# Kernel tuning notes

Hardware: AMD Instinct MI355X
Metric: run time of the kernel (lower is better)

## Reference

```python
import jax, jax.numpy as jnp
import numpy as np

B, S, D, H = 8, 2048, 64, 4
Dh = D // H  # head_dim = 16


def setup_inputs() -> dict:
    key = jax.random.key(0)
    k1, k2, k3, k4 = jax.random.split(key, 4)
    x = jax.random.normal(k1, (B, S, D), jnp.float32)
    # Linear weights stored torch-style as [out_features, in_features]
    W_qkv = jax.random.normal(k2, (3 * D, D), jnp.float32) * 0.125
    W_proj = jax.random.normal(k3, (D, D), jnp.float32) * 0.125
    b_proj = jnp.zeros((D,), jnp.float32)
    # Ragged structure: random valid length per sample, causal + padding mask
    lens = jax.random.randint(k4, (B,), S // 4, S + 1)
    pos = jnp.arange(S)
    key_valid = pos[None, :] < lens[:, None]          # [B, S]
    causal = pos[:, None] >= pos[None, :]             # [S, S]
    attn_mask = (causal[None, :, :] & key_valid[:, None, :])[:, None, :, :]  # [B,1,S,S], True=attend
    return {"x": x, "attn_mask": attn_mask, "W_qkv": W_qkv, "W_proj": W_proj, "b_proj": b_proj}


def reference(x, attn_mask, W_qkv, W_proj, b_proj):
    b, s, d = x.shape
    # fused QKV projection (qkv_bias=False)
    qkv = x @ W_qkv.T                                  # [B, S, 3D]
    qkv = qkv.reshape(b, s, 3, H, Dh).transpose(2, 0, 3, 1, 4)  # [3, B, H, S, Dh]
    q, k, v = qkv[0], qkv[1], qkv[2]
    scale = 1.0 / jnp.sqrt(jnp.asarray(Dh, x.dtype))
    scores = jnp.einsum('bhqd,bhkd->bhqk', q, k) * scale  # [B, H, S, S]
    neg = jnp.asarray(jnp.finfo(scores.dtype).min, scores.dtype)
    scores = jnp.where(attn_mask, scores, neg)
    attn = jax.nn.softmax(scores, axis=-1)
    ctx = jnp.einsum('bhqk,bhkd->bhqd', attn, v)       # [B, H, S, Dh]
    ctx = ctx.transpose(0, 2, 1, 3).reshape(b, s, d)   # [B, S, D]
    return ctx @ W_proj.T + b_proj
```

## Files before the change

### kernel.cpp

```cpp
#include <hip/hip_runtime.h>
#include <hip/hip_bf16.h>

typedef __attribute__((ext_vector_type(4))) float f32x4;
typedef __attribute__((ext_vector_type(16))) float f32x16;
typedef __attribute__((ext_vector_type(8))) short bf16x8;
typedef __attribute__((ext_vector_type(4))) short bf16x4;

#define SEQ 2048
#define NH 4
#define DH 16

#define WS_LEN 0
#define WS_WP  1024
#define WS_Q   65536
#define WS_K   (WS_Q + 2097152)
#define WS_V   (WS_K + 2097152)

#define MFMA16 __builtin_amdgcn_mfma_f32_16x16x32_bf16
#define MFMA32 __builtin_amdgcn_mfma_f32_32x32x16_bf16

__device__ __forceinline__ short f2bf(float f){
  __hip_bfloat16 h = __float2bfloat16(f);
  return __builtin_bit_cast(short, h);
}

__device__ __forceinline__ bf16x8 pack8(f32x4 a, f32x4 b){
  bf16x8 r;
  r[0]=f2bf(a[0]); r[1]=f2bf(a[1]); r[2]=f2bf(a[2]); r[3]=f2bf(a[3]);
  r[4]=f2bf(b[0]); r[5]=f2bf(b[1]); r[6]=f2bf(b[2]); r[7]=f2bf(b[3]);
  return r;
}

__global__ __launch_bounds__(256) void qkv_prep_kernel(const float* __restrict__ x,
                                                       const unsigned char* __restrict__ mask,
                                                       const float* __restrict__ wqkv,
                                                       const float* __restrict__ wproj,
                                                       unsigned char* __restrict__ ws){
  const int tid = threadIdx.x;
  if (blockIdx.x == 256){
    if (blockIdx.y == 1){
      short* wp = (short*)(ws + WS_WP);
      for (int i = tid; i < 64*64; i += 256) wp[i] = f2bf(wproj[i]);
      return;
    }
    const unsigned w0 = *(const unsigned*)mask;
    const int mode = (mask[2048] != 0) ? 0 : ((w0 == 1u) ? 1 : ((w0 == 0x3f800000u) ? 2 : 0));
    __shared__ int cnts[8];
    if (tid < 8) cnts[tid] = 0;
    __syncthreads();
    const int b = tid >> 5, j = tid & 31;
    const long long rowbase = (long long)b * SEQ * SEQ + (long long)(SEQ-1) * SEQ;
    int c = 0;
    if (mode == 0){
      const unsigned* mw = (const unsigned*)(mask + rowbase);
      for (int k = j; k < SEQ/4; k += 32){
        unsigned v = mw[k];
        c += (v & 0xffu ? 1:0) + (v & 0xff00u ? 1:0) + (v & 0xff0000u ? 1:0) + (v & 0xff000000u ? 1:0);
      }
    } else if (mode == 1){
      for (int k = j; k < SEQ; k += 32) c += ((const int*)mask)[rowbase + k] != 0;
    } else {
      for (int k = j; k < SEQ; k += 32) c += ((const float*)mask)[rowbase + k] != 0.0f;
    }
    atomicAdd(&cnts[b], c);
    __syncthreads();
    if (tid < 8) ((int*)ws)[tid] = cnts[tid];
    return;
  }

  const int lane = tid & 63;
  const int wv   = tid >> 6;
  const int c    = lane & 15;
  const int g    = lane >> 4;
  const int T0   = blockIdx.x * 64 + wv * 16;
  const f32x4 z = {0.f, 0.f, 0.f, 0.f};

  bf16x8 aw[2];
  {
    const float* xr = x + (long long)(T0 + c) * 64 + g * 8;
    #pragma unroll
    for (int w = 0; w < 2; ++w){
      f32x4 lo = *(const f32x4*)(xr + w*32);
      f32x4 hi = *(const f32x4*)(xr + w*32 + 4);
      aw[w] = pack8(lo, hi);
    }
  }

  const int tokbase = T0 + g*4;
  const int b = tokbase >> 11;
  const int sbase = tokbase & (SEQ-1);
  short* Qd = (short*)(ws + WS_Q);
  short* Kd = (short*)(ws + WS_K);
  short* Vd = (short*)(ws + WS_V);

  #pragma unroll
  for (int oi = 0; oi < 6; ++oi){
    const int ot = blockIdx.y * 6 + oi;
    const float* wr = wqkv + (ot*16 + c) * 64 + g * 8;
    bf16x8 b0 = pack8(*(const f32x4*)(wr),      *(const f32x4*)(wr + 4));
    bf16x8 b1 = pack8(*(const f32x4*)(wr + 32), *(const f32x4*)(wr + 36));
    f32x4 acc = z;
    acc = MFMA16(aw[0], b0, acc, 0, 0, 0);
    acc = MFMA16(aw[1], b1, acc, 0, 0, 0);
    if (ot < 4){
      short* dst = Qd + ((long long)(b*NH + ot) * SEQ) * DH + c;
      #pragma unroll
      for (int r = 0; r < 4; ++r)
        dst[(long long)(sbase + r) * DH] = f2bf(acc[r] * (0.25f * 1.44269504f));
    } else if (ot < 8){
      short* dst = Kd + ((long long)(b*NH + (ot-4)) * SEQ) * DH + c;
      #pragma unroll
      for (int r = 0; r < 4; ++r)
        dst[(long long)(sbase + r) * DH] = f2bf(acc[r]);
    } else {
      bf16x4 pk;
      #pragma unroll
      for (int r = 0; r < 4; ++r) pk[r] = f2bf(acc[r]);
      *(bf16x4*)(Vd + ((long long)(b*NH + (ot-8)) * DH + c) * SEQ + sbase) = pk;
    }
  }
}

__global__ __launch_bounds__(512, 4) void attn_kernel(const unsigned char* __restrict__ ws,
                                                      const float* __restrict__ bproj,
                                                      float* __restrict__ out){
  const int tid  = threadIdx.x;
  const int lane = tid & 63;
  const int wv   = tid >> 6;
  const int h    = wv & 3;
  const int half = wv >> 2;
  const int c    = lane & 15;
  const int g    = lane >> 4;
  const int ql   = lane & 31;
  const int hi   = lane >> 5;
  const int L    = blockIdx.x;
  const int b    = L & 7;
  const int u    = L >> 3;
  const int t    = (u < 32) ? (2*u) : (63 - 2*(u - 32));
  const int q0   = t * 32;
  const int len  = ((const int*)ws)[b];
  const long long bh = (long long)(b*NH + h);
  const short* Q  = (const short*)(ws + WS_Q) + bh * SEQ * DH;
  const short* K  = (const short*)(ws + WS_K) + bh * SEQ * DH;
  const short* Vt = (const short*)(ws + WS_V) + bh * DH * SEQ;
  const short* Wp = (const short*)(ws + WS_WP);

  __shared__ __align__(16) unsigned char smem[78848];
  float* CMB = (float*)(smem + 65536);
  float* LSB = (float*)(smem + 74240);
  const unsigned pb   = (unsigned)wv * 8192;
  const unsigned CTXB = 74752;
  const f32x4 z  = {0.f,0.f,0.f,0.f};
  const f32x16 z16 = {0.f,0.f,0.f,0.f,0.f,0.f,0.f,0.f,0.f,0.f,0.f,0.f,0.f,0.f,0.f,0.f};

  const bf16x8 qf = *(const bf16x8*)(Q + (q0 + ql)*DH + hi*8);

  f32x4 acc[2] = {z, z};
  f32x4 lsv = z;
  const int kcount = min(q0 + 32, len);
  const int nkt  = (kcount + 63) >> 6;
  const int icnt = min(q0 >> 6, len >> 6);
  const int nh0  = nkt >> 1;
  const int kb   = half ? nh0 : 0;
  const int ke   = half ? nkt : nh0;
  const int qg   = q0 + ql;
  const unsigned swq  = (unsigned)(ql & 7) << 4;
  const unsigned sw   = (unsigned)(c & 7) << 4;

  auto qkexp = [&](int tt, bf16x8 (&kk)[2]){
    const int k0 = tt * 64;
    const bool nomask = tt < icnt;
    const unsigned rowb = pb + ((unsigned)(tt & 1) << 12) + (unsigned)ql*128;
    #pragma unroll
    for (int kb32 = 0; kb32 < 2; ++kb32){
      f32x16 st = MFMA32(kk[kb32], qf, z16, 0, 0, 0);
      #pragma unroll
      for (int grp = 0; grp < 4; ++grp){
        const int keybase = kb32*32 + grp*8 + hi*4;
        float p0, p1, p2, p3;
        {
          float e0 = __builtin_amdgcn_exp2f(st[grp*4 + 0]);
          float e1 = __builtin_amdgcn_exp2f(st[grp*4 + 1]);
          float e2 = __builtin_amdgcn_exp2f(st[grp*4 + 2]);
          float e3 = __builtin_amdgcn_exp2f(st[grp*4 + 3]);
          if (!nomask){
            const int k = k0 + keybase;
            e0 = (k   <= qg && k   < len) ? e0 : 0.f;
            e1 = (k+1 <= qg && k+1 < len) ? e1 : 0.f;
            e2 = (k+2 <= qg && k+2 < len) ? e2 : 0.f;
            e3 = (k+3 <= qg && k+3 < len) ? e3 : 0.f;
          }
          p0 = e0; p1 = e1; p2 = e2; p3 = e3;
        }
        lsv[0] += p0; lsv[1] += p1; lsv[2] += p2; lsv[3] += p3;
        uint2 pk;
        pk.x = __builtin_amdgcn_perm(__builtin_bit_cast(unsigned, p1),
                                     __builtin_bit_cast(unsigned, p0), 0x07060302u);
        pk.y = __builtin_amdgcn_perm(__builtin_bit_cast(unsigned, p3),
                                     __builtin_bit_cast(unsigned, p2), 0x07060302u);
        *(uint2*)&smem[rowb + ((unsigned)(keybase*2) ^ swq)] = pk;
      }
    }
  };

  bf16x8 knx[2], vcur[2], vnx[2], knn[2], vnn[2];
  if (kb < ke){
    const int k0 = kb * 64;
    bf16x8 k0f[2];
    k0f[0] = *(const bf16x8*)(K + (k0 + ql)*DH + hi*8);
    k0f[1] = *(const bf16x8*)(K + (k0 + 32 + ql)*DH + hi*8);
    vcur[0] = *(const bf16x8*)(Vt + c*SEQ + k0 + g*8);
    vcur[1] = *(const bf16x8*)(Vt + c*SEQ + k0 + 32 + g*8);
    qkexp(kb, k0f);
    if (kb + 1 < ke){
      const int k1 = k0 + 64;
      knx[0] = *(const bf16x8*)(K + (k1 + ql)*DH + hi*8);
      knx[1] = *(const bf16x8*)(K + (k1 + 32 + ql)*DH + hi*8);
      vnx[0] = *(const bf16x8*)(Vt + c*SEQ + k1 + g*8);
      vnx[1] = *(const bf16x8*)(Vt + c*SEQ + k1 + 32 + g*8);
    }
  }

  for (int kt = kb; kt < ke; ++kt){
    const unsigned bufr = pb + ((unsigned)(kt & 1) << 12);
    bf16x8 pa[2][2];
    #pragma unroll
    for (int qb = 0; qb < 2; ++qb)
      #pragma unroll
      for (int w = 0; w < 2; ++w)
        pa[qb][w] = *(const bf16x8*)&smem[bufr + (qb*16 + c)*128 + ((unsigned)(w*64 + g*16) ^ sw)];

    if (kt + 1 < ke){
      if (kt + 2 < ke){
        const int k2 = (kt + 2) * 64;
        knn[0] = *(const bf16x8*)(K + (k2 + ql)*DH + hi*8);
        knn[1] = *(const bf16x8*)(K + (k2 + 32 + ql)*DH + hi*8);
        vnn[0] = *(const bf16x8*)(Vt + c*SEQ + k2 + g*8);
        vnn[1] = *(const bf16x8*)(Vt + c*SEQ + k2 + 32 + g*8);
      }
      qkexp(kt + 1, knx);
    }

    #pragma unroll
    for (int qb = 0; qb < 2; ++qb)
      #pragma unroll
      for (int w = 0; w < 2; ++w)
        acc[qb] = MFMA16(pa[qb][w], vcur[w], acc[qb], 0, 0, 0);

    vcur[0] = vnx[0]; vcur[1] = vnx[1];
    knx[0] = knn[0]; knx[1] = knn[1];
    vnx[0] = vnn[0]; vnx[1] = vnn[1];
  }

  float ls = lsv[0] + lsv[1] + lsv[2] + lsv[3];
  ls += __shfl_xor(ls, 32);

  if (half == 0){
    #pragma unroll
    for (int qb = 0; qb < 2; ++qb)
      #pragma unroll
      for (int r = 0; r < 4; ++r)
        CMB[(h*32 + qb*16 + g*4 + r)*17 + c] = acc[qb][r];
    if (lane < 32) LSB[h*32 + lane] = ls;
  }
  __syncthreads();
  if (half == 1){
    #pragma unroll
    for (int qb = 0; qb < 2; ++qb){
      #pragma unroll
      for (int r = 0; r < 4; ++r){
        const int q = qb*16 + g*4 + r;
        const float tot = acc[qb][r] + CMB[(h*32 + q)*17 + c];
        const float lsT = LSB[h*32 + q] + __shfl(ls, q);
        const float cv  = tot / lsT;
        *(short*)&smem[CTXB + q*128 +
            (((unsigned)((h*16 + c)*2)) ^ ((unsigned)(q & 7) << 4))] = f2bf(cv);
      }
    }
  }
  __syncthreads();

  bf16x8 wpf[2];
  #pragma unroll
  for (int w = 0; w < 2; ++w)
    wpf[w] = *(const bf16x8*)(Wp + (h*16 + c)*64 + w*32 + g*8);
  const float bias = bproj[h*16 + c];
  f32x4 oa = z;
  const unsigned rbc = CTXB + (half*16 + c)*128;
  #pragma unroll
  for (int w = 0; w < 2; ++w){
    bf16x8 pa = *(const bf16x8*)&smem[rbc + ((unsigned)(w*64 + g*16) ^ sw)];
    oa = MFMA16(pa, wpf[w], oa, 0, 0, 0);
  }
  #pragma unroll
  for (int r = 0; r < 4; ++r)
    out[((long long)b * SEQ + q0 + half*16 + g*4 + r) * 64 + h*16 + c] = oa[r] + bias;
}

extern "C" void kernel_launch(void* const* d_in, const int* in_sizes, int n_in,
                              void* d_out, int out_size, void* d_ws, size_t ws_size,
                              hipStream_t stream) {
  const float* x     = (const float*)d_in[0];
  const unsigned char* mask = (const unsigned char*)d_in[1];
  const float* wqkv  = (const float*)d_in[2];
  const float* wproj = (const float*)d_in[3];
  const float* bproj = (const float*)d_in[4];
  float* out = (float*)d_out;
  unsigned char* ws = (unsigned char*)d_ws;

  qkv_prep_kernel<<<dim3(257, 2), 256, 0, stream>>>(x, mask, wqkv, wproj, ws);
  attn_kernel<<<512, 512, 0, stream>>>(ws, bproj, out);
}
```

Before: 35.70 us.

## Compute softmax row sums via MFMA with ones vector and rotate batch mapping

Replaces the per-lane VALU accumulation of exponentials with an extra MFMA that multiplies the bf16 probability tile by a ones vector, so the row sums come out of the matrix core in the same layout as the context accumulator. This drops the fp32 adds and the cross-lane shuffles. It also means the denominator is summed from bf16-rounded probabilities, which matches the numerator. Separately, the block-to-batch mapping is rotated by L>>8 to spread ragged-length batches across the grid differently. The cost is doubling the MFMA count in the PV step.

```diff
diff --git a/kernel.cpp b/kernel.cpp
--- a/kernel.cpp
+++ b/kernel.cpp
@@ -134,7 +134,7 @@
   const int ql   = lane & 31;
   const int hi   = lane >> 5;
   const int L    = blockIdx.x;
-  const int b    = L & 7;
+  const int b    = (L + (L >> 8)) & 7;
   const int u    = L >> 3;
   const int t    = (u < 32) ? (2*u) : (63 - 2*(u - 32));
   const int q0   = t * 32;
@@ -152,11 +152,13 @@
   const unsigned CTXB = 74752;
   const f32x4 z  = {0.f,0.f,0.f,0.f};
   const f32x16 z16 = {0.f,0.f,0.f,0.f,0.f,0.f,0.f,0.f,0.f,0.f,0.f,0.f,0.f,0.f,0.f,0.f};
+  const short one_bf = (short)0x3F80;
+  const bf16x8 ones = {one_bf,one_bf,one_bf,one_bf,one_bf,one_bf,one_bf,one_bf};
 
   const bf16x8 qf = *(const bf16x8*)(Q + (q0 + ql)*DH + hi*8);
 
-  f32x4 acc[2] = {z, z};
-  f32x4 lsv = z;
+  f32x4 acc[2]  = {z, z};
+  f32x4 accS[2] = {z, z};
   const int kcount = min(q0 + 32, len);
   const int nkt  = (kcount + 63) >> 6;
   const int icnt = min(q0 >> 6, len >> 6);
@@ -177,22 +179,17 @@
       #pragma unroll
       for (int grp = 0; grp < 4; ++grp){
         const int keybase = kb32*32 + grp*8 + hi*4;
-        float p0, p1, p2, p3;
-        {
-          float e0 = __builtin_amdgcn_exp2f(st[grp*4 + 0]);
-          float e1 = __builtin_amdgcn_exp2f(st[grp*4 + 1]);
-          float e2 = __builtin_amdgcn_exp2f(st[grp*4 + 2]);
-          float e3 = __builtin_amdgcn_exp2f(st[grp*4 + 3]);
-          if (!nomask){
-            const int k = k0 + keybase;
-            e0 = (k   <= qg && k   < len) ? e0 : 0.f;
-            e1 = (k+1 <= qg && k+1 < len) ? e1 : 0.f;
-            e2 = (k+2 <= qg && k+2 < len) ? e2 : 0.f;
-            e3 = (k+3 <= qg && k+3 < len) ? e3 : 0.f;
-          }
-          p0 = e0; p1 = e1; p2 = e2; p3 = e3;
+        float p0 = __builtin_amdgcn_exp2f(st[grp*4 + 0]);
+        float p1 = __builtin_amdgcn_exp2f(st[grp*4 + 1]);
+        float p2 = __builtin_amdgcn_exp2f(st[grp*4 + 2]);
+        float p3 = __builtin_amdgcn_exp2f(st[grp*4 + 3]);
+        if (!nomask){
+          const int k = k0 + keybase;
+          p0 = (k   <= qg && k   < len) ? p0 : 0.f;
+          p1 = (k+1 <= qg && k+1 < len) ? p1 : 0.f;
+          p2 = (k+2 <= qg && k+2 < len) ? p2 : 0.f;
+          p3 = (k+3 <= qg && k+3 < len) ? p3 : 0.f;
         }
-        lsv[0] += p0; lsv[1] += p1; lsv[2] += p2; lsv[3] += p3;
         uint2 pk;
         pk.x = __builtin_amdgcn_perm(__builtin_bit_cast(unsigned, p1),
                                      __builtin_bit_cast(unsigned, p0), 0x07060302u);
@@ -244,24 +241,28 @@
     #pragma unroll
     for (int qb = 0; qb < 2; ++qb)
       #pragma unroll
-      for (int w = 0; w < 2; ++w)
-        acc[qb] = MFMA16(pa[qb][w], vcur[w], acc[qb], 0, 0, 0);
+      for (int w = 0; w < 2; ++w){
+        acc[qb]  = MFMA16(pa[qb][w], vcur[w], acc[qb], 0, 0, 0);
+        accS[qb] = MFMA16(pa[qb][w], ones,    accS[qb], 0, 0, 0);
+      }
 
     vcur[0] = vnx[0]; vcur[1] = vnx[1];
     knx[0] = knn[0]; knx[1] = knn[1];
     vnx[0] = vnn[0]; vnx[1] = vnn[1];
   }
 
-  float ls = lsv[0] + lsv[1] + lsv[2] + lsv[3];
-  ls += __shfl_xor(ls, 32);
-
   if (half == 0){
     #pragma unroll
-    for (int qb = 0; qb < 2; ++qb)
+    for (int qb = 0; qb < 2; ++qb){
       #pragma unroll
       for (int r = 0; r < 4; ++r)
         CMB[(h*32 + qb*16 + g*4 + r)*17 + c] = acc[qb][r];
-    if (lane < 32) LSB[h*32 + lane] = ls;
+      if (c == 0){
+        #pragma unroll
+        for (int r = 0; r < 4; ++r)
+          LSB[h*32 + qb*16 + g*4 + r] = accS[qb][r];
+      }
+    }
   }
   __syncthreads();
   if (half == 1){
@@ -271,7 +272,7 @@
       for (int r = 0; r < 4; ++r){
         const int q = qb*16 + g*4 + r;
         const float tot = acc[qb][r] + CMB[(h*32 + q)*17 + c];
-        const float lsT = LSB[h*32 + q] + __shfl(ls, q);
+        const float lsT = LSB[h*32 + q] + accS[qb][r];
         const float cv  = tot / lsT;
         *(short*)&smem[CTXB + q*128 +
             (((unsigned)((h*16 + c)*2)) ^ ((unsigned)(q & 7) << 4))] = f2bf(cv);
```

New measurement: 32.18 us. 1.11x faster.
